# Performance work log

Hardware: AMD Instinct MI355X
Metric: run time of the kernel (lower is better)

The kernel has to match this reference:

```python
import jax, jax.numpy as jnp
import numpy as np

EMBED = 1024
HEADS = 16
HDIM = EMBED // HEADS
QLEN = 512
KLEN = 1024
BATCH = 8


def setup_inputs() -> dict:
    key = jax.random.key(0)
    ks = jax.random.split(key, 20)
    s = 0.02
    return {
        "query": jax.random.normal(ks[0], (QLEN, BATCH, EMBED), jnp.float32),
        "key": jax.random.normal(ks[1], (KLEN, BATCH, EMBED), jnp.float32),
        "value": jax.random.normal(ks[2], (KLEN, BATCH, EMBED), jnp.float32),
        "pos_embedding": jax.random.normal(ks[3], (KLEN, 1, EMBED), jnp.float32),
        "U": jax.random.normal(ks[4], (HEADS, HDIM), jnp.float32) * s,
        "V": jax.random.normal(ks[5], (HEADS, HDIM), jnp.float32) * s,
        "mask": jax.random.randint(ks[6], (QLEN, KLEN, 1), 0, 2) == 1,
        "padding_mask": jax.random.randint(ks[7], (BATCH, QLEN), 0, 2).astype(jnp.float32),
        "Wq": jax.random.normal(ks[8], (EMBED, EMBED), jnp.float32) * s,
        "bq": jnp.zeros((EMBED,), jnp.float32),
        "Wk": jax.random.normal(ks[9], (EMBED, EMBED), jnp.float32) * s,
        "bk": jnp.zeros((EMBED,), jnp.float32),
        "Wv": jax.random.normal(ks[10], (EMBED, EMBED), jnp.float32) * s,
        "bv": jnp.zeros((EMBED,), jnp.float32),
        "Wpos": jax.random.normal(ks[11], (EMBED, EMBED), jnp.float32) * s,
        "Wo": jax.random.normal(ks[12], (EMBED, EMBED), jnp.float32) * s,
        "bo": jnp.zeros((EMBED,), jnp.float32),
    }


def _rel_shift(x):
    # x: (q, k, b, h) -> Transformer-XL relative shift (pad/reshape trick)
    q, k, b, h = x.shape
    zero_pad = jnp.zeros((q, 1, b, h), x.dtype)
    x_padded = jnp.concatenate([zero_pad, x], axis=1)  # (q, k+1, b, h)
    x_padded = x_padded.reshape(k + 1, q, b, h)
    return x_padded[1:].reshape(q, k, b, h)


def _padding_mask(pad, q_len, k_len):
    # pad: (b, q) in {0,1}; returns bool (b, q, k) where True = masked
    pm = jnp.einsum('bq,bk->bqk', pad, pad)  # (b, q, q)
    if k_len > q_len:
        mem = jnp.ones((pad.shape[0], q_len, k_len - q_len), pad.dtype)
        pm = jnp.concatenate([mem, pm], axis=2)
    return pm == 0


def reference(query, key, value, pos_embedding, U, V, mask, padding_mask,
              Wq, bq, Wk, bk, Wv, bv, Wpos, Wo, bo):
    q_len, b, e = query.shape
    k_len = key.shape[0]
    d = jnp.asarray(np.sqrt(e), query.dtype)

    q = (query @ Wq + bq).reshape(q_len, b, HEADS, HDIM)
    k = (key @ Wk + bk).reshape(k_len, b, HEADS, HDIM)
    v = (value @ Wv + bv).reshape(k_len, b, HEADS, HDIM)
    R = (pos_embedding @ Wpos).reshape(-1, HEADS, HDIM)  # (k_len, h, d)

    content = jnp.einsum('qbhd,kbhd->qkbh', q + U, k)
    position = _rel_shift(jnp.einsum('qbhd,khd->qkbh', q + V, R))
    score = (content + position) / d  # (q, k, b, h)

    NEG = jnp.asarray(-1e20, score.dtype)
    score = jnp.where(mask[:, :, :, None], NEG, score)  # mask (q,k,1)->(q,k,1,1)
    pmask = _padding_mask(padding_mask, q_len, k_len)  # (b,q,k)
    pmask = jnp.transpose(pmask, (1, 2, 0))[:, :, :, None]  # (q,k,b,1)
    score = jnp.where(pmask, NEG, score)

    attn = jax.nn.softmax(score, axis=1)
    alpha = jnp.einsum('qkbh,kbhd->qbhd', attn, v).reshape(q_len, b, e)
    return alpha @ Wo + bo
```

## Files before the change

kernel.cpp:

```cpp
#include <hip/hip_runtime.h>

#define QLEN 512
#define KLEN 1024
#define BATCH 8
#define HEADS 16
#define HDIM 64
#define EMBED 1024

typedef __attribute__((ext_vector_type(4))) float f32x4;
typedef __attribute__((ext_vector_type(8))) short short8;
typedef unsigned short ushort_t;
typedef unsigned char uchar_t;
typedef unsigned int uint_t;

#define MFMA16(a, b, c) __builtin_amdgcn_mfma_f32_16x16x32_bf16((a), (b), (c), 0, 0, 0)

__device__ __forceinline__ float b2f(ushort_t u) {
    union { uint_t i; float f; } c; c.i = ((uint_t)u) << 16; return c.f;
}
__device__ __forceinline__ ushort_t f2b(float x) {
    union { float f; uint_t i; } c; c.f = x;
    return (ushort_t)((c.i + 0x8000u) >> 16);
}
__device__ __forceinline__ uint_t pk2(float lo, float hi) {
    return (uint_t)f2b(lo) | ((uint_t)f2b(hi) << 16);
}
__device__ __forceinline__ float ldf(const void* p, int idx, int f32m) {
    if (f32m) return ((const float*)p)[idx];
    return b2f(((const ushort_t*)p)[idx]);
}

typedef const __attribute__((address_space(1))) void async_src_t;
typedef __attribute__((address_space(3))) void async_dst_t;

__global__ __launch_bounds__(256) void detect_kernel(const void* mask, const void* pad, int* flags) {
    __shared__ int cnt[4];
    int tid = threadIdx.x;
    if (tid < 4) cnt[tid] = 0;
    __syncthreads();
    const uchar_t* mb = (const uchar_t*)mask;
    const uchar_t* pb = (const uchar_t*)pad;
    int lnz1 = 0, l3f1 = 0, l3f3 = 0, lpnz = 0;
    for (int off = tid; off < 4096; off += 256) {
        uchar_t v = mb[off];
        int m4 = off & 3;
        if (m4 != 0 && v != 0) lnz1++;
        if (m4 == 1 && v == 0x3F) l3f1++;
        if (m4 == 3 && v == 0x3F) l3f3++;
        uchar_t p = pb[off];
        if (m4 == 0 && p != 0) lpnz++;
    }
    atomicAdd(&cnt[0], lnz1); atomicAdd(&cnt[1], l3f1);
    atomicAdd(&cnt[2], l3f3); atomicAdd(&cnt[3], lpnz);
    __syncthreads();
    if (tid == 0) {
        flags[0] = (cnt[3] == 0) ? 1 : 0;
        int mm;
        if (cnt[0] == 0) mm = 0;
        else if (cnt[1] > 16) mm = 2;
        else if (cnt[2] > 16) mm = 3;
        else mm = 1;
        flags[1] = mm;
    }
}

__global__ __launch_bounds__(256) void convert_kernel(const void* __restrict__ src,
                                                      ushort_t* __restrict__ dst,
                                                      int n8, const int* flags) {
    int i = blockIdx.x * 256 + threadIdx.x;
    if (i >= n8) return;
    if (flags[0]) {
        const float4* s = (const float4*)src + (size_t)i * 2;
        float4 a = s[0], b = s[1];
        uint4 o;
        o.x = pk2(a.x, a.y); o.y = pk2(a.z, a.w);
        o.z = pk2(b.x, b.y); o.w = pk2(b.z, b.w);
        ((uint4*)dst)[i] = o;
    } else {
        ((uint4*)dst)[i] = ((const uint4*)src)[i];
    }
}

__global__ __launch_bounds__(256) void maskprep_kernel(const void* __restrict__ mask,
                                                       const void* __restrict__ pad,
                                                       uint_t* __restrict__ bits,
                                                       const int* flags) {
    int tid = blockIdx.x * 256 + threadIdx.x;
    int w = tid & 31, q = (tid >> 5) & 511, b = tid >> 14;
    int mm = flags[1], f32m = flags[0];
    float padq = ldf(pad, b * 512 + q, f32m);
    uint_t word = 0;
    for (int j = 0; j < 32; ++j) {
        int k = w * 32 + j;
        size_t mi = (size_t)q * 1024 + k;
        int dead;
        if (mm == 1) dead = (((const uchar_t*)mask)[mi] != 0);
        else if (mm == 2) dead = (((const ushort_t*)mask)[mi] != 0);
        else dead = (((const uint_t*)mask)[mi] != 0);
        if (k >= 512) {
            float padk = ldf(pad, b * 512 + k - 512, f32m);
            if (padq == 0.f || padk == 0.f) dead = 1;
        }
        word |= ((uint_t)dead) << j;
    }
    bits[((b * 8 + (w >> 2)) * 512 + q) * 4 + (w & 3)] = word;
}

__global__ __launch_bounds__(256) void transpose_kernel(
    const void* W0, const void* W1, const void* W2, const void* W3, const void* W4,
    ushort_t* T0, ushort_t* T1, ushort_t* T2, ushort_t* T3, ushort_t* T4,
    const int* flags) {
    __shared__ float tl[32][33];
    int f32m = flags[0];
    const void* W; ushort_t* T;
    switch (blockIdx.z) {
        case 0: W = W0; T = T0; break;
        case 1: W = W1; T = T1; break;
        case 2: W = W2; T = T2; break;
        case 3: W = W3; T = T3; break;
        default: W = W4; T = T4; break;
    }
    int tx = threadIdx.x, ty = threadIdx.y;
    int x = blockIdx.x * 32 + tx;
    #pragma unroll
    for (int j = 0; j < 4; ++j) {
        int row = blockIdx.y * 32 + ty + j * 8;
        tl[ty + j * 8][tx] = ldf(W, row * 1024 + x, f32m);
    }
    __syncthreads();
    #pragma unroll
    for (int j = 0; j < 4; ++j) {
        int n = blockIdx.x * 32 + ty + j * 8;
        T[n * 1024 + blockIdx.y * 32 + tx] = f2b(tl[tx][ty + j * 8]);
    }
}

__global__ __launch_bounds__(256) void vtrans_kernel(const ushort_t* __restrict__ vh,
                                                     ushort_t* __restrict__ vT) {
    __shared__ ushort_t t[64][68];
    int bh = blockIdx.y;
    int k0 = blockIdx.x * 64;
    int tid = threadIdx.x;
    int r = tid >> 2, c0 = (tid & 3) * 16;
    const short8* src = (const short8*)&vh[((size_t)bh * 1024 + k0 + r) * 64 + c0];
    *(short8*)&t[r][c0] = src[0];
    *(short8*)&t[r][c0 + 8] = src[1];
    __syncthreads();
    ushort_t tmp[16];
    #pragma unroll
    for (int j = 0; j < 16; ++j) tmp[j] = t[c0 + j][r];
    int dm = r >> 4, cc = r & 15;
    #pragma unroll
    for (int tt = 0; tt < 2; ++tt) {
        int og = ((k0 + c0) >> 3) + tt;
        int kc = og >> 4, ch = (og >> 2) & 3, g = og & 3;
        size_t addr = ((((((size_t)bh * 8 + kc) * 4 + ch) * 4 + dm) * 64) + cc * 4 + g) * 8;
        *(short8*)&vT[addr] = *(short8*)&tmp[tt * 8];
    }
}

template<int EPI>
__global__ __launch_bounds__(256) void gemm_kernel(
    const void* Av, const ushort_t* BT, int M,
    const void* bias, const void* Up, const void* Vp,
    void* out0, void* out1, const int* flags, int a_mode) {
    __shared__ ushort_t As[4096];
    __shared__ ushort_t Bs[4096];
    const int f32m = flags[0];
    const int a_f32 = a_mode ? f32m : 0;
    const int tid = threadIdx.x;
    const int wid = tid >> 6, lane = tid & 63;
    const int wr = (wid >> 1) * 64, wc = (wid & 1) * 64;
    const int m0 = blockIdx.x * 128, n0 = blockIdx.y * 128;
    const int ch0 = wid * 2;
    const int lrow = lane >> 2, lcol = (lane & 3) * 8;

    f32x4 acc[4][4];
    #pragma unroll
    for (int m = 0; m < 4; ++m)
        #pragma unroll
        for (int n = 0; n < 4; ++n)
            acc[m][n] = (f32x4){0.f, 0.f, 0.f, 0.f};

    for (int k0 = 0; k0 < 1024; k0 += 32) {
        if (a_f32) {
            const float* Af = (const float*)Av + (size_t)(m0 + (tid >> 1)) * 1024 + k0 + (tid & 1) * 16;
            ushort_t* dst = &As[(tid >> 1) * 32 + (tid & 1) * 16];
            #pragma unroll
            for (int e = 0; e < 16; ++e) dst[e] = f2b(Af[e]);
        } else {
            #pragma unroll
            for (int t = 0; t < 2; ++t) {
                int ch = ch0 + t;
                const ushort_t* ga = (const ushort_t*)Av + (size_t)(m0 + ch * 16 + lrow) * 1024 + k0 + lcol;
                __builtin_amdgcn_global_load_lds((async_src_t*)ga, (async_dst_t*)&As[ch * 512], 16, 0, 0);
            }
        }
        #pragma unroll
        for (int t = 0; t < 2; ++t) {
            int ch = ch0 + t;
            const ushort_t* gb = BT + (size_t)(n0 + ch * 16 + lrow) * 1024 + k0 + lcol;
            __builtin_amdgcn_global_load_lds((async_src_t*)gb, (async_dst_t*)&Bs[ch * 512], 16, 0, 0);
        }
        __syncthreads();

        short8 af[4], bf[4];
        #pragma unroll
        for (int m = 0; m < 4; ++m)
            af[m] = *(const short8*)&As[(wr + m * 16 + (lane & 15)) * 32 + (lane >> 4) * 8];
        #pragma unroll
        for (int n = 0; n < 4; ++n)
            bf[n] = *(const short8*)&Bs[(wc + n * 16 + (lane & 15)) * 32 + (lane >> 4) * 8];
        #pragma unroll
        for (int m = 0; m < 4; ++m)
            #pragma unroll
            for (int n = 0; n < 4; ++n)
                acc[m][n] = MFMA16(af[m], bf[n], acc[m][n]);
        __syncthreads();
    }

    #pragma unroll
    for (int n = 0; n < 4; ++n) {
        int gn = n0 + wc + n * 16 + (lane & 15);
        float bv_ = (EPI == 2) ? 0.f : ldf(bias, gn, f32m);
        float uu = 0.f, vv = 0.f;
        if (EPI == 0) { uu = ldf(Up, gn, f32m); vv = ldf(Vp, gn, f32m); }
        #pragma unroll
        for (int m = 0; m < 4; ++m) {
            #pragma unroll
            for (int j = 0; j < 4; ++j) {
                int gm = m0 + wr + m * 16 + (lane >> 4) * 4 + j;
                float c = acc[m][n][j] + bv_;
                if (EPI == 0) {
                    int q = gm >> 3, b = gm & 7;
                    int h = gn >> 6, d = gn & 63;
                    int bhk = b * 16 + h;
                    size_t addr = ((size_t)bhk * 32 + (q >> 4)) * 1024 + (size_t)(d >> 5) * 512
                                  + ((q & 15) * 4 + ((d >> 3) & 3)) * 8 + (d & 7);
                    ((ushort_t*)out0)[addr] = f2b((c + uu) * 0.03125f);
                    ((ushort_t*)out1)[addr] = f2b((c + vv) * 0.03125f);
                } else if (EPI == 1) {
                    int kk = gm >> 3, b = gm & 7;
                    int h = gn >> 6, d = gn & 63;
                    ((ushort_t*)out0)[((b * 16 + h) * 1024 + kk) * 64 + d] = f2b(c);
                } else if (EPI == 2) {
                    int h = gn >> 6, d = gn & 63;
                    int jr = gm;
                    size_t addr = (((((size_t)h * 8 + (jr >> 7)) * 8 + ((jr >> 4) & 7)) * 2 + (d >> 5)) * 64
                                   + ((jr & 15) * 4 + ((d >> 3) & 3))) * 8 + (d & 7);
                    ((ushort_t*)out0)[addr] = f2b(c);
                } else if (EPI == 4) {
                    int kk = gm >> 3, b = gm & 7;
                    int h = gn >> 6, d = gn & 63;
                    size_t addr = ((((((size_t)(b * 16 + h)) * 8 + (kk >> 7)) * 8 + ((kk >> 4) & 7)) * 2 + (d >> 5)) * 64
                                   + ((kk & 15) * 4 + ((d >> 3) & 3))) * 8 + (d & 7);
                    ((ushort_t*)out0)[addr] = f2b(c);
                } else {
                    if (f32m) ((float*)out0)[gm * 1024 + gn] = c;
                    else ((ushort_t*)out0)[gm * 1024 + gn] = f2b(c);
                }
            }
        }
    }
}

#define SP_STR 1032
#define PB_STR 136
__global__ __launch_bounds__(512, 4) void attn_kernel(
    const ushort_t* __restrict__ qU, const ushort_t* __restrict__ qV,
    const ushort_t* __restrict__ khn, const ushort_t* __restrict__ vtn,
    const ushort_t* __restrict__ Rln, const uint_t* __restrict__ mbits,
    ushort_t* __restrict__ alpha) {

    __shared__ __align__(16) uchar_t uni[35104];
    ushort_t* sPos = (ushort_t*)uni;
    ushort_t* sPb  = (ushort_t*)uni;
    float*    sO   = (float*)uni;
    __shared__ float sred[2][8][16];
    __shared__ float ssinv[16];

    const int tid = threadIdx.x;
    const int wid = tid >> 6, lane = tid & 63;
    const int g = lane >> 4, c = lane & 15;
    const int qt = blockIdx.x;
    const int q0 = qt * 16;
    const int bh = blockIdx.y;
    const int b = bh >> 4, h = bh & 15;
    const int kbase = wid * 128;
    const int lch = (c * 4 + g) * 8;

    {
        size_t qvb = ((size_t)bh * 32 + qt) * 1024;
        short8 bva0 = *(const short8*)&qV[qvb + lch];
        short8 bva1 = *(const short8*)&qV[qvb + 512 + lch];
        int qtb = (qt == 31) ? 31 : qt + 1;
        int cb = (qt == 31) ? 15 : c;
        size_t qvb2 = ((size_t)bh * 32 + qtb) * 1024;
        short8 bvb0 = *(const short8*)&qV[qvb2 + (cb * 4 + g) * 8];
        short8 bvb1 = *(const short8*)&qV[qvb2 + 512 + (cb * 4 + g) * 8];
        #pragma unroll
        for (int m = 0; m < 8; ++m) {
            size_t rb = ((((size_t)h * 8 + wid) * 8 + m) * 2) * 512;
            short8 ra0 = *(const short8*)&Rln[rb + lch];
            short8 ra1 = *(const short8*)&Rln[rb + 512 + lch];
            f32x4 p0 = (f32x4){0.f, 0.f, 0.f, 0.f};
            p0 = MFMA16(ra0, bva0, p0);
            p0 = MFMA16(ra1, bva1, p0);
            f32x4 p1 = (f32x4){0.f, 0.f, 0.f, 0.f};
            p1 = MFMA16(ra0, bvb0, p1);
            p1 = MFMA16(ra1, bvb1, p1);
            uint2 w;
            w.x = pk2(p0[0], p0[1]);
            w.y = pk2(p0[2], p0[3]);
            *(uint2*)&sPos[c * SP_STR + kbase + m * 16 + g * 4] = w;
            if (c == 0) {
                uint2 x;
                x.x = pk2(p1[0], p1[1]);
                x.y = pk2(p1[2], p1[3]);
                *(uint2*)&sPos[16 * SP_STR + kbase + m * 16 + g * 4] = x;
            }
        }
    }

    f32x4 acc[8];
    {
        size_t qub = ((size_t)bh * 32 + qt) * 1024;
        short8 bu0 = *(const short8*)&qU[qub + lch];
        short8 bu1 = *(const short8*)&qU[qub + 512 + lch];
        #pragma unroll
        for (int m = 0; m < 8; ++m) {
            size_t kb = ((((size_t)bh * 8 + wid) * 8 + m) * 2) * 512;
            short8 ka0 = *(const short8*)&khn[kb + lch];
            short8 ka1 = *(const short8*)&khn[kb + 512 + lch];
            f32x4 t = (f32x4){0.f, 0.f, 0.f, 0.f};
            t = MFMA16(ka0, bu0, t);
            t = MFMA16(ka1, bu1, t);
            acc[m] = t;
        }
    }
    __syncthreads();

    const int q = q0 + c;
    uint4 mw = *(const uint4*)(mbits + ((size_t)(b * 8 + wid) * 512 + q) * 4);
    uint_t mwa[4] = {mw.x, mw.y, mw.z, mw.w};

    float mx = -3.0e38f;
    #pragma unroll
    for (int m = 0; m < 8; ++m) {
        int k0e = kbase + m * 16 + g * 4;
        uint_t word = mwa[m >> 1];
        #pragma unroll
        for (int jj = 0; jj < 4; ++jj) {
            int k = k0e + jj;
            int delta = k - q;
            int wrap = (delta > 512) ? 1 : 0;
            int j = wrap ? (delta - 514) : (delta + 511);
            float pos = b2f(sPos[(c + wrap) * SP_STR + (j < 0 ? 0 : j)]);
            if (delta == 513) pos = 0.f;
            float s = acc[m][jj] + pos;
            if ((word >> ((m & 1) * 16 + g * 4 + jj)) & 1u) s = -1e20f;
            acc[m][jj] = s;
            mx = fmaxf(mx, s);
        }
    }
    mx = fmaxf(mx, __shfl_xor(mx, 16, 64));
    mx = fmaxf(mx, __shfl_xor(mx, 32, 64));
    if (lane < 16) sred[0][wid][c] = mx;
    __syncthreads();
    {
        float a0 = fmaxf(fmaxf(sred[0][0][c], sred[0][1][c]), fmaxf(sred[0][2][c], sred[0][3][c]));
        float a1 = fmaxf(fmaxf(sred[0][4][c], sred[0][5][c]), fmaxf(sred[0][6][c], sred[0][7][c]));
        mx = fmaxf(a0, a1);
    }

    float ls = 0.f;
    #pragma unroll
    for (int m = 0; m < 8; ++m) {
        float p0 = __expf(acc[m][0] - mx);
        float p1 = __expf(acc[m][1] - mx);
        float p2 = __expf(acc[m][2] - mx);
        float p3 = __expf(acc[m][3] - mx);
        ls += (p0 + p1) + (p2 + p3);
        uint2 w;
        w.x = pk2(p0, p1);
        w.y = pk2(p2, p3);
        *(uint2*)&sPb[(wid * 16 + c) * PB_STR + m * 16 + g * 4] = w;
    }
    ls += __shfl_xor(ls, 16, 64);
    ls += __shfl_xor(ls, 32, 64);
    if (lane < 16) sred[1][wid][c] = ls;

    short8 va[4][4];
    #pragma unroll
    for (int ch = 0; ch < 4; ++ch)
        #pragma unroll
        for (int dm = 0; dm < 4; ++dm)
            va[ch][dm] = *(const short8*)&vtn[((((((size_t)bh * 8 + wid) * 4 + ch) * 4 + dm) * 64) * 8) + lch];
    __syncthreads();
    float ls2;
    {
        float a0 = (sred[1][0][c] + sred[1][1][c]) + (sred[1][2][c] + sred[1][3][c]);
        float a1 = (sred[1][4][c] + sred[1][5][c]) + (sred[1][6][c] + sred[1][7][c]);
        ls2 = a0 + a1;
    }
    if (wid == 0 && lane < 16) ssinv[c] = 1.0f / ls2;

    f32x4 oacc[4];
    #pragma unroll
    for (int dm = 0; dm < 4; ++dm) oacc[dm] = (f32x4){0.f, 0.f, 0.f, 0.f};
    short8 pbv[4];
    #pragma unroll
    for (int ch = 0; ch < 4; ++ch)
        pbv[ch] = *(const short8*)&sPb[(wid * 16 + c) * PB_STR + ch * 32 + g * 8];
    #pragma unroll
    for (int ch = 0; ch < 4; ++ch)
        #pragma unroll
        for (int dm = 0; dm < 4; ++dm)
            oacc[dm] = MFMA16(va[ch][dm], pbv[ch], oacc[dm]);

    __syncthreads();
    #pragma unroll
    for (int dm = 0; dm < 4; ++dm)
        #pragma unroll
        for (int jj = 0; jj < 4; ++jj)
            sO[wid * 1088 + (dm * 16 + g * 4 + jj) * 17 + c] = oacc[dm][jj];
    __syncthreads();
    for (int e = tid; e < 1024; e += 512) {
        int d = e & 63, qq = e >> 6;
        float v = ((sO[d * 17 + qq] + sO[1088 + d * 17 + qq]) +
                   (sO[2176 + d * 17 + qq] + sO[3264 + d * 17 + qq])) +
                  ((sO[4352 + d * 17 + qq] + sO[5440 + d * 17 + qq]) +
                   (sO[6528 + d * 17 + qq] + sO[7616 + d * 17 + qq]));
        v *= ssinv[qq];
        alpha[((size_t)(q0 + qq) * 8 + b) * 1024 + h * 64 + d] = f2b(v);
    }
}

extern "C" void kernel_launch(void* const* d_in, const int* in_sizes, int n_in,
                              void* d_out, int out_size, void* d_ws, size_t ws_size,
                              hipStream_t stream) {
    char* ws = (char*)d_ws;
    int* flags = (int*)ws;
    ushort_t* WqT   = (ushort_t*)(ws + 1024);
    ushort_t* WkT   = WqT + 1048576;
    ushort_t* WvT   = WkT + 1048576;
    ushort_t* WposT = WvT + 1048576;
    ushort_t* WoT   = WposT + 1048576;
    ushort_t* qUw   = WoT + 1048576;
    ushort_t* qVw   = qUw + 4194304;
    ushort_t* khw   = qVw + 4194304;
    ushort_t* Rlw   = khw + 8388608;
    ushort_t* R1    = Rlw + 1048576;
    ushort_t* R2    = R1 + 4194304;
    ushort_t* R3    = R2 + 8388608;
    ushort_t* qbf = R1;
    ushort_t* alw = R1;
    ushort_t* kbf = R2;
    ushort_t* vhw = R2;
    ushort_t* vbf = R3;
    ushort_t* vTw = R3;
    uint_t* mbits = (uint_t*)WqT;
    ushort_t* pbf = WvT;

    detect_kernel<<<1, 256, 0, stream>>>(d_in[6], d_in[7], flags);
    convert_kernel<<<2048, 256, 0, stream>>>(d_in[0], qbf, 524288, flags);
    convert_kernel<<<4096, 256, 0, stream>>>(d_in[1], kbf, 1048576, flags);
    convert_kernel<<<4096, 256, 0, stream>>>(d_in[2], vbf, 1048576, flags);
    transpose_kernel<<<dim3(32, 32, 5), dim3(32, 8), 0, stream>>>(
        d_in[8], d_in[10], d_in[12], d_in[14], d_in[15],
        WqT, WkT, WvT, WposT, WoT, flags);
    gemm_kernel<0><<<dim3(32, 8), 256, 0, stream>>>(qbf, WqT, 4096, d_in[9], d_in[4], d_in[5], qUw, qVw, flags, 0);
    maskprep_kernel<<<512, 256, 0, stream>>>(d_in[6], d_in[7], mbits, flags);
    gemm_kernel<4><<<dim3(64, 8), 256, 0, stream>>>(kbf, WkT, 8192, d_in[11], nullptr, nullptr, khw, nullptr, flags, 0);
    gemm_kernel<1><<<dim3(64, 8), 256, 0, stream>>>(vbf, WvT, 8192, d_in[13], nullptr, nullptr, vhw, nullptr, flags, 0);
    convert_kernel<<<512, 256, 0, stream>>>(d_in[3], pbf, 131072, flags);
    gemm_kernel<2><<<dim3(8, 8), 256, 0, stream>>>(pbf, WposT, 1024, nullptr, nullptr, nullptr, Rlw, nullptr, flags, 0);
    vtrans_kernel<<<dim3(16, 128), 256, 0, stream>>>(vhw, vTw);
    attn_kernel<<<dim3(32, 128), 512, 0, stream>>>(qUw, qVw, khw, vTw, Rlw, mbits, alw);
    gemm_kernel<3><<<dim3(32, 8), 256, 0, stream>>>(alw, WoT, 4096, d_in[16], nullptr, nullptr, d_out, nullptr, flags, 0);
}
```

Before: 330.3 us.

## Merge prep, projection and pre-attention launches and specialize position-bias indexing

Folds the three input conversions and the five weight transposes into one launch. The Q, K and pos projection GEMMs go into a single multi-role launch, and the V transpose and mask-bit preparation share another. This cuts the launch count from thirteen to six, which reduces launch gaps and tail effects on small grids. The pos GEMM now converts fp32 input inline instead of running a separate conversion pass. In the attention kernel, the relative-shift position lookup gets fast paths for 16-wide tiles that lie entirely on one side of the wrap, removing per-element branching. The cost is larger branching kernels that may have worse register use, and the mask prep now runs after the V GEMM.

```diff
diff --git a/kernel.cpp b/kernel.cpp
--- a/kernel.cpp
+++ b/kernel.cpp
@@ -64,12 +64,10 @@
     }
 }
 
-__global__ __launch_bounds__(256) void convert_kernel(const void* __restrict__ src,
-                                                      ushort_t* __restrict__ dst,
-                                                      int n8, const int* flags) {
-    int i = blockIdx.x * 256 + threadIdx.x;
+__device__ __forceinline__ void conv_body(const void* __restrict__ src, ushort_t* __restrict__ dst,
+                                          int i, int n8, int f32m) {
     if (i >= n8) return;
-    if (flags[0]) {
+    if (f32m) {
         const float4* s = (const float4*)src + (size_t)i * 2;
         float4 a = s[0], b = s[1];
         uint4 o;
@@ -81,97 +79,62 @@
     }
 }
 
-__global__ __launch_bounds__(256) void maskprep_kernel(const void* __restrict__ mask,
-                                                       const void* __restrict__ pad,
-                                                       uint_t* __restrict__ bits,
-                                                       const int* flags) {
-    int tid = blockIdx.x * 256 + threadIdx.x;
-    int w = tid & 31, q = (tid >> 5) & 511, b = tid >> 14;
-    int mm = flags[1], f32m = flags[0];
-    float padq = ldf(pad, b * 512 + q, f32m);
-    uint_t word = 0;
-    for (int j = 0; j < 32; ++j) {
-        int k = w * 32 + j;
-        size_t mi = (size_t)q * 1024 + k;
-        int dead;
-        if (mm == 1) dead = (((const uchar_t*)mask)[mi] != 0);
-        else if (mm == 2) dead = (((const ushort_t*)mask)[mi] != 0);
-        else dead = (((const uint_t*)mask)[mi] != 0);
-        if (k >= 512) {
-            float padk = ldf(pad, b * 512 + k - 512, f32m);
-            if (padq == 0.f || padk == 0.f) dead = 1;
-        }
-        word |= ((uint_t)dead) << j;
-    }
-    bits[((b * 8 + (w >> 2)) * 512 + q) * 4 + (w & 3)] = word;
-}
-
-__global__ __launch_bounds__(256) void transpose_kernel(
+__global__ __launch_bounds__(256) void prep_kernel(
+    const void* q_in, ushort_t* qbf, const void* k_in, ushort_t* kbf,
+    const void* v_in, ushort_t* vbf,
     const void* W0, const void* W1, const void* W2, const void* W3, const void* W4,
     ushort_t* T0, ushort_t* T1, ushort_t* T2, ushort_t* T3, ushort_t* T4,
     const int* flags) {
     __shared__ float tl[32][33];
-    int f32m = flags[0];
-    const void* W; ushort_t* T;
-    switch (blockIdx.z) {
-        case 0: W = W0; T = T0; break;
-        case 1: W = W1; T = T1; break;
-        case 2: W = W2; T = T2; break;
-        case 3: W = W3; T = T3; break;
-        default: W = W4; T = T4; break;
-    }
-    int tx = threadIdx.x, ty = threadIdx.y;
-    int x = blockIdx.x * 32 + tx;
-    #pragma unroll
-    for (int j = 0; j < 4; ++j) {
-        int row = blockIdx.y * 32 + ty + j * 8;
-        tl[ty + j * 8][tx] = ldf(W, row * 1024 + x, f32m);
-    }
-    __syncthreads();
-    #pragma unroll
-    for (int j = 0; j < 4; ++j) {
-        int n = blockIdx.x * 32 + ty + j * 8;
-        T[n * 1024 + blockIdx.y * 32 + tx] = f2b(tl[tx][ty + j * 8]);
-    }
-}
-
-__global__ __launch_bounds__(256) void vtrans_kernel(const ushort_t* __restrict__ vh,
-                                                     ushort_t* __restrict__ vT) {
-    __shared__ ushort_t t[64][68];
-    int bh = blockIdx.y;
-    int k0 = blockIdx.x * 64;
-    int tid = threadIdx.x;
-    int r = tid >> 2, c0 = (tid & 3) * 16;
-    const short8* src = (const short8*)&vh[((size_t)bh * 1024 + k0 + r) * 64 + c0];
-    *(short8*)&t[r][c0] = src[0];
-    *(short8*)&t[r][c0 + 8] = src[1];
-    __syncthreads();
-    ushort_t tmp[16];
-    #pragma unroll
-    for (int j = 0; j < 16; ++j) tmp[j] = t[c0 + j][r];
-    int dm = r >> 4, cc = r & 15;
-    #pragma unroll
-    for (int tt = 0; tt < 2; ++tt) {
-        int og = ((k0 + c0) >> 3) + tt;
-        int kc = og >> 4, ch = (og >> 2) & 3, g = og & 3;
-        size_t addr = ((((((size_t)bh * 8 + kc) * 4 + ch) * 4 + dm) * 64) + cc * 4 + g) * 8;
-        *(short8*)&vT[addr] = *(short8*)&tmp[tt * 8];
+    const int bid = blockIdx.x;
+    const int tid = threadIdx.x;
+    const int f32m = flags[0];
+    if (bid < 2048) {
+        conv_body(q_in, qbf, bid * 256 + tid, 524288, f32m);
+    } else if (bid < 6144) {
+        conv_body(k_in, kbf, (bid - 2048) * 256 + tid, 1048576, f32m);
+    } else if (bid < 10240) {
+        conv_body(v_in, vbf, (bid - 6144) * 256 + tid, 1048576, f32m);
+    } else {
+        int l = bid - 10240;
+        int z = l >> 10, r = l & 1023;
+        int bx = r & 31, by = r >> 5;
+        const void* W; ushort_t* T;
+        switch (z) {
+            case 0: W = W0; T = T0; break;
+            case 1: W = W1; T = T1; break;
+            case 2: W = W2; T = T2; break;
+            case 3: W = W3; T = T3; break;
+            default: W = W4; T = T4; break;
+        }
+        int tx = tid & 31, ty = tid >> 5;
+        int x = bx * 32 + tx;
+        #pragma unroll
+        for (int j = 0; j < 4; ++j) {
+            int row = by * 32 + ty + j * 8;
+            tl[ty + j * 8][tx] = ldf(W, row * 1024 + x, f32m);
+        }
+        __syncthreads();
+        #pragma unroll
+        for (int j = 0; j < 4; ++j) {
+            int n = bx * 32 + ty + j * 8;
+            T[n * 1024 + by * 32 + tx] = f2b(tl[tx][ty + j * 8]);
+        }
     }
 }
 
 template<int EPI>
-__global__ __launch_bounds__(256) void gemm_kernel(
-    const void* Av, const ushort_t* BT, int M,
+__device__ __forceinline__ void gemm_body(
+    int mt, int nt, const void* Av, const ushort_t* BT,
     const void* bias, const void* Up, const void* Vp,
-    void* out0, void* out1, const int* flags, int a_mode) {
-    __shared__ ushort_t As[4096];
-    __shared__ ushort_t Bs[4096];
+    void* out0, void* out1, const int* flags, int a_mode,
+    ushort_t* As, ushort_t* Bs) {
     const int f32m = flags[0];
     const int a_f32 = a_mode ? f32m : 0;
     const int tid = threadIdx.x;
     const int wid = tid >> 6, lane = tid & 63;
     const int wr = (wid >> 1) * 64, wc = (wid & 1) * 64;
-    const int m0 = blockIdx.x * 128, n0 = blockIdx.y * 128;
+    const int m0 = mt * 128, n0 = nt * 128;
     const int ch0 = wid * 2;
     const int lrow = lane >> 2, lcol = (lane & 3) * 8;
 
@@ -264,6 +227,85 @@
     }
 }
 
+template<int EPI>
+__global__ __launch_bounds__(256) void gemm_kernel(
+    const void* Av, const ushort_t* BT, int M,
+    const void* bias, const void* Up, const void* Vp,
+    void* out0, void* out1, const int* flags, int a_mode) {
+    __shared__ ushort_t As[4096];
+    __shared__ ushort_t Bs[4096];
+    gemm_body<EPI>(blockIdx.x, blockIdx.y, Av, BT, bias, Up, Vp, out0, out1, flags, a_mode, As, Bs);
+}
+
+__global__ __launch_bounds__(256) void proj1_kernel(
+    const ushort_t* qbf, const ushort_t* WqT, const void* bq, const void* Up, const void* Vp,
+    ushort_t* qUw, ushort_t* qVw,
+    const ushort_t* kbf, const ushort_t* WkT, const void* bk, ushort_t* khw,
+    const void* pos_raw, const ushort_t* WposT, ushort_t* Rlw,
+    const int* flags) {
+    __shared__ ushort_t As[4096];
+    __shared__ ushort_t Bs[4096];
+    const int bid = blockIdx.x;
+    if (bid < 256) {
+        gemm_body<0>(bid & 31, bid >> 5, qbf, WqT, bq, Up, Vp, qUw, qVw, flags, 0, As, Bs);
+    } else if (bid < 768) {
+        int l = bid - 256;
+        gemm_body<4>(l & 63, l >> 6, kbf, WkT, bk, nullptr, nullptr, khw, nullptr, flags, 0, As, Bs);
+    } else {
+        int l = bid - 768;
+        gemm_body<2>(l & 7, l >> 3, pos_raw, WposT, nullptr, nullptr, nullptr, Rlw, nullptr, flags, 1, As, Bs);
+    }
+}
+
+__global__ __launch_bounds__(256) void preattn_kernel(
+    const ushort_t* __restrict__ vh, ushort_t* __restrict__ vT,
+    const void* __restrict__ mask, const void* __restrict__ pad,
+    uint_t* __restrict__ bits, const int* flags) {
+    __shared__ ushort_t t[64][68];
+    const int bid = blockIdx.x;
+    const int tid = threadIdx.x;
+    if (bid < 2048) {
+        int bh = bid >> 4;
+        int k0 = (bid & 15) * 64;
+        int r = tid >> 2, c0 = (tid & 3) * 16;
+        const short8* src = (const short8*)&vh[((size_t)bh * 1024 + k0 + r) * 64 + c0];
+        *(short8*)&t[r][c0] = src[0];
+        *(short8*)&t[r][c0 + 8] = src[1];
+        __syncthreads();
+        ushort_t tmp[16];
+        #pragma unroll
+        for (int j = 0; j < 16; ++j) tmp[j] = t[c0 + j][r];
+        int dm = r >> 4, cc = r & 15;
+        #pragma unroll
+        for (int tt = 0; tt < 2; ++tt) {
+            int og = ((k0 + c0) >> 3) + tt;
+            int kc = og >> 4, ch = (og >> 2) & 3, g = og & 3;
+            size_t addr = ((((((size_t)bh * 8 + kc) * 4 + ch) * 4 + dm) * 64) + cc * 4 + g) * 8;
+            *(short8*)&vT[addr] = *(short8*)&tmp[tt * 8];
+        }
+    } else {
+        int tid2 = (bid - 2048) * 256 + tid;
+        int w = tid2 & 31, q = (tid2 >> 5) & 511, b = tid2 >> 14;
+        int mm = flags[1], f32m = flags[0];
+        float padq = ldf(pad, b * 512 + q, f32m);
+        uint_t word = 0;
+        for (int j = 0; j < 32; ++j) {
+            int k = w * 32 + j;
+            size_t mi = (size_t)q * 1024 + k;
+            int dead;
+            if (mm == 1) dead = (((const uchar_t*)mask)[mi] != 0);
+            else if (mm == 2) dead = (((const ushort_t*)mask)[mi] != 0);
+            else dead = (((const uint_t*)mask)[mi] != 0);
+            if (k >= 512) {
+                float padk = ldf(pad, b * 512 + k - 512, f32m);
+                if (padq == 0.f || padk == 0.f) dead = 1;
+            }
+            word |= ((uint_t)dead) << j;
+        }
+        bits[((b * 8 + (w >> 2)) * 512 + q) * 4 + (w & 3)] = word;
+    }
+}
+
 #define SP_STR 1032
 #define PB_STR 136
 __global__ __launch_bounds__(512, 4) void attn_kernel(
@@ -344,23 +386,43 @@
     uint4 mw = *(const uint4*)(mbits + ((size_t)(b * 8 + wid) * 512 + q) * 4);
     uint_t mwa[4] = {mw.x, mw.y, mw.z, mw.w};
 
+    const int mbase = kbase - q0;
     float mx = -3.0e38f;
     #pragma unroll
     for (int m = 0; m < 8; ++m) {
-        int k0e = kbase + m * 16 + g * 4;
+        const int mb = mbase + m * 16;
         uint_t word = mwa[m >> 1];
-        #pragma unroll
-        for (int jj = 0; jj < 4; ++jj) {
-            int k = k0e + jj;
-            int delta = k - q;
-            int wrap = (delta > 512) ? 1 : 0;
-            int j = wrap ? (delta - 514) : (delta + 511);
-            float pos = b2f(sPos[(c + wrap) * SP_STR + (j < 0 ? 0 : j)]);
-            if (delta == 513) pos = 0.f;
-            float s = acc[m][jj] + pos;
-            if ((word >> ((m & 1) * 16 + g * 4 + jj)) & 1u) s = -1e20f;
-            acc[m][jj] = s;
-            mx = fmaxf(mx, s);
+        if (mb + 15 <= 512) {
+            int a0 = c * SP_STR + mb + g * 4 - c + 511;
+            #pragma unroll
+            for (int jj = 0; jj < 4; ++jj) {
+                float s = acc[m][jj] + b2f(sPos[a0 + jj]);
+                if ((word >> ((m & 1) * 16 + g * 4 + jj)) & 1u) s = -1e20f;
+                acc[m][jj] = s;
+                mx = fmaxf(mx, s);
+            }
+        } else if (mb - 15 >= 514) {
+            int a0 = (c + 1) * SP_STR + mb + g * 4 - c - 514;
+            #pragma unroll
+            for (int jj = 0; jj < 4; ++jj) {
+                float s = acc[m][jj] + b2f(sPos[a0 + jj]);
+                if ((word >> ((m & 1) * 16 + g * 4 + jj)) & 1u) s = -1e20f;
+                acc[m][jj] = s;
+                mx = fmaxf(mx, s);
+            }
+        } else {
+            #pragma unroll
+            for (int jj = 0; jj < 4; ++jj) {
+                int delta = mb + g * 4 + jj - c;
+                int wrap = (delta > 512) ? 1 : 0;
+                int j = wrap ? (delta - 514) : (delta + 511);
+                float pos = b2f(sPos[(c + wrap) * SP_STR + j]);
+                if (delta == 513) pos = 0.f;
+                float s = acc[m][jj] + pos;
+                if ((word >> ((m & 1) * 16 + g * 4 + jj)) & 1u) s = -1e20f;
+                acc[m][jj] = s;
+                mx = fmaxf(mx, s);
+            }
         }
     }
     mx = fmaxf(mx, __shfl_xor(mx, 16, 64));
@@ -460,22 +522,18 @@
     ushort_t* vbf = R3;
     ushort_t* vTw = R3;
     uint_t* mbits = (uint_t*)WqT;
-    ushort_t* pbf = WvT;
 
     detect_kernel<<<1, 256, 0, stream>>>(d_in[6], d_in[7], flags);
-    convert_kernel<<<2048, 256, 0, stream>>>(d_in[0], qbf, 524288, flags);
-    convert_kernel<<<4096, 256, 0, stream>>>(d_in[1], kbf, 1048576, flags);
-    convert_kernel<<<4096, 256, 0, stream>>>(d_in[2], vbf, 1048576, flags);
-    transpose_kernel<<<dim3(32, 32, 5), dim3(32, 8), 0, stream>>>(
+    prep_kernel<<<15360, 256, 0, stream>>>(
+        d_in[0], qbf, d_in[1], kbf, d_in[2], vbf,
         d_in[8], d_in[10], d_in[12], d_in[14], d_in[15],
         WqT, WkT, WvT, WposT, WoT, flags);
-    gemm_kernel<0><<<dim3(32, 8), 256, 0, stream>>>(qbf, WqT, 4096, d_in[9], d_in[4], d_in[5], qUw, qVw, flags, 0);
-    maskprep_kernel<<<512, 256, 0, stream>>>(d_in[6], d_in[7], mbits, flags);
-    gemm_kernel<4><<<dim3(64, 8), 256, 0, stream>>>(kbf, WkT, 8192, d_in[11], nullptr, nullptr, khw, nullptr, flags, 0);
+    proj1_kernel<<<832, 256, 0, stream>>>(
+        qbf, WqT, d_in[9], d_in[4], d_in[5], qUw, qVw,
+        kbf, WkT, d_in[11], khw,
+        d_in[3], WposT, Rlw, flags);
     gemm_kernel<1><<<dim3(64, 8), 256, 0, stream>>>(vbf, WvT, 8192, d_in[13], nullptr, nullptr, vhw, nullptr, flags, 0);
-    convert_kernel<<<512, 256, 0, stream>>>(d_in[3], pbf, 131072, flags);
-    gemm_kernel<2><<<dim3(8, 8), 256, 0, stream>>>(pbf, WposT, 1024, nullptr, nullptr, nullptr, Rlw, nullptr, flags, 0);
-    vtrans_kernel<<<dim3(16, 128), 256, 0, stream>>>(vhw, vTw);
+    preattn_kernel<<<2560, 256, 0, stream>>>(vhw, vTw, d_in[6], d_in[7], mbits, flags);
     attn_kernel<<<dim3(32, 128), 512, 0, stream>>>(qUw, qVw, khw, vTw, Rlw, mbits, alw);
     gemm_kernel<3><<<dim3(32, 8), 256, 0, stream>>>(alw, WoT, 4096, d_in[16], nullptr, nullptr, d_out, nullptr, flags, 0);
 }
```

After: 316.6 us, median of 2. -4.1%, faster.
